# Optimization experiments

Measured on AMD Instinct MI355X. Metric: run time of the kernel, lower is better.

Reference implementation:

```python
import jax, jax.numpy as jnp
import numpy as np

B, H, W, C = 64, 28, 28, 384
NH, WS = 12, 7
KD = C // NH            # key_dim = head_dim = 32 (attn_ratio=1.0 -> d = KD)
QKV_OUT = 3 * KD * NH   # 1152
HID = 4 * C             # mlp hidden
N = WS * WS             # tokens per window
L = H * W
SCALE = KD ** -0.5
EPS_LN = 1e-5
EPS_BN = 1e-5


def _make_bias_idxs():
    pts = [(i, j) for i in range(WS) for j in range(WS)]
    offs, idxs = {}, []
    for p1 in pts:
        for p2 in pts:
            o = (abs(p1[0] - p2[0]), abs(p1[1] - p2[1]))
            if o not in offs:
                offs[o] = len(offs)
            idxs.append(offs[o])
    return np.asarray(idxs, dtype=np.int32).reshape(N, N)


def _ln(x, g, b):
    m = jnp.mean(x, axis=-1, keepdims=True)
    v = jnp.mean(jnp.square(x - m), axis=-1, keepdims=True)
    return (x - m) * jax.lax.rsqrt(v + EPS_LN) * g + b


def setup_inputs() -> dict:
    key = jax.random.key(0)
    ks = jax.random.split(key, 8)
    s = 0.02
    return {
        "x": jax.random.normal(ks[0], (B, L, C), jnp.float32),
        "ln_a_g": jnp.ones((C,), jnp.float32),
        "ln_a_b": jnp.zeros((C,), jnp.float32),
        "qkv_w": jax.random.normal(ks[1], (QKV_OUT, C), jnp.float32) * s,
        "qkv_b": jnp.zeros((QKV_OUT,), jnp.float32),
        "attn_bias": jax.random.normal(ks[2], (NH, N), jnp.float32) * s,
        "proj_w": jax.random.normal(ks[3], (C, C), jnp.float32) * s,
        "proj_b": jnp.zeros((C,), jnp.float32),
        "conv_w": jax.random.normal(ks[4], (C, 1, 3, 3), jnp.float32) * s,
        "bn_g": jnp.ones((C,), jnp.float32),
        "bn_b": jnp.zeros((C,), jnp.float32),
        "bn_m": jnp.zeros((C,), jnp.float32),
        "bn_v": jnp.ones((C,), jnp.float32),
        "ln_m_g": jnp.ones((C,), jnp.float32),
        "ln_m_b": jnp.zeros((C,), jnp.float32),
        "fc1_w": jax.random.normal(ks[5], (HID, C), jnp.float32) * s,
        "fc1_b": jnp.zeros((HID,), jnp.float32),
        "fc2_w": jax.random.normal(ks[6], (C, HID), jnp.float32) * s,
        "fc2_b": jnp.zeros((C,), jnp.float32),
        "bias_idxs": jnp.asarray(_make_bias_idxs()),
    }


def reference(x, ln_a_g, ln_a_b, qkv_w, qkv_b, attn_bias, proj_w, proj_b,
              conv_w, bn_g, bn_b, bn_m, bn_v, ln_m_g, ln_m_b,
              fc1_w, fc1_b, fc2_w, fc2_b, bias_idxs):
    res = x
    nh, nw = H // WS, W // WS
    # window partition: [B,L,C] -> [B*nWin, N, C]
    xw = x.reshape(B, nh, WS, nw, WS, C).transpose(0, 1, 3, 2, 4, 5)
    xw = xw.reshape(B * nh * nw, N, C)
    # attention
    xn = _ln(xw, ln_a_g, ln_a_b)
    qkv = xn @ qkv_w.T + qkv_b                       # [Bw, N, 3*NH*KD]
    qkv = qkv.reshape(-1, N, NH, 3 * KD).transpose(0, 2, 1, 3)
    q, k, v = qkv[..., :KD], qkv[..., KD:2 * KD], qkv[..., 2 * KD:]
    bias = attn_bias[:, bias_idxs]                   # [NH, N, N]
    attn = jnp.einsum('bhnd,bhmd->bhnm', q, k) * SCALE + bias
    attn = jax.nn.softmax(attn, axis=-1)
    o = jnp.einsum('bhnm,bhmd->bhnd', attn, v)
    o = o.transpose(0, 2, 1, 3).reshape(-1, N, C)
    o = o @ proj_w.T + proj_b
    # window unpartition -> [B, L, C]
    o = o.reshape(B, nh, nw, WS, WS, C).transpose(0, 1, 3, 2, 4, 5).reshape(B, L, C)
    x = res + o
    # depthwise ConvBN (inference BN)
    xc = x.transpose(0, 2, 1).reshape(B, C, H, W)
    xc = jax.lax.conv_general_dilated(
        xc, conv_w, (1, 1), 'SAME', feature_group_count=C,
        dimension_numbers=('NCHW', 'OIHW', 'NCHW'))
    inv = jax.lax.rsqrt(bn_v + EPS_BN)
    xc = (xc - bn_m[None, :, None, None]) * (bn_g * inv)[None, :, None, None] + bn_b[None, :, None, None]
    x = xc.reshape(B, C, L).transpose(0, 2, 1)
    # MLP residual
    h = _ln(x, ln_m_g, ln_m_b)
    h = jax.nn.gelu(h @ fc1_w.T + fc1_b, approximate=False)
    h = h @ fc2_w.T + fc2_b
    return x + h
```

## Files before the change

kernel.cpp:

```cpp
#include <hip/hip_runtime.h>
#include <hip/hip_bf16.h>
#include <stdint.h>

#define BATCH 64
#define CC 384
#define NHEAD 12
#define KD 32
#define NTOK 49
#define LL 784
#define MTOT 50176
#define HID 1536
#define QKV_OUT 1152
#define SCALE 0.17677669529663687f
#define EPS 1e-5f

typedef __bf16 bf16x8 __attribute__((ext_vector_type(8)));
typedef float f32x4 __attribute__((ext_vector_type(4)));

__device__ __forceinline__ float bf2f(unsigned short u) {
  union { unsigned int u; float f; } cv; cv.u = ((unsigned int)u) << 16; return cv.f;
}
__device__ __forceinline__ unsigned short f2bf(float f) {
  union { float f; unsigned int u; } cv; cv.f = f;
  unsigned int r = cv.u + 0x7FFFu + ((cv.u >> 16) & 1u);
  return (unsigned short)(r >> 16);
}
__device__ __forceinline__ void gl_lds16(const unsigned short* g, unsigned short* l) {
  __builtin_amdgcn_global_load_lds(
      (const __attribute__((address_space(1))) unsigned int*)g,
      (__attribute__((address_space(3))) unsigned int*)l, 16, 0, 0);
}

__global__ void detect_kernel(const unsigned short* __restrict__ x, int* flag) {
  __shared__ int cnt;
  if (threadIdx.x == 0) cnt = 0;
  __syncthreads();
  int c = 0;
  for (int i = threadIdx.x; i < 4096; i += 256) {
    if (((x[i] >> 7) & 0xFF) == 0xFF) c++;
  }
  atomicAdd(&cnt, c);
  __syncthreads();
  if (threadIdx.x == 0) *flag = (cnt > 0) ? 1 : 0;
}

struct CvtArgs {
  const void* src[19];
  unsigned int n[19];
  unsigned int off[19];
};
__global__ __launch_bounds__(256) void convert_kernel(
    CvtArgs a, unsigned short* __restrict__ dst, const int* __restrict__ flag) {
  const int which = blockIdx.y;
  const unsigned int nn = a.n[which];
  unsigned short* d = dst + a.off[which];
  const unsigned int stride = gridDim.x * blockDim.x;
  const unsigned int idx = blockIdx.x * blockDim.x + threadIdx.x;
  const unsigned int ng = nn >> 3;
  if (*flag) {
    const float* s = (const float*)a.src[which];
    for (unsigned int g = idx; g < ng; g += stride) {
      const float4 f0 = ((const float4*)s)[g * 2];
      const float4 f1 = ((const float4*)s)[g * 2 + 1];
      ushort4 lo, hi;
      lo.x = f2bf(f0.x); lo.y = f2bf(f0.y); lo.z = f2bf(f0.z); lo.w = f2bf(f0.w);
      hi.x = f2bf(f1.x); hi.y = f2bf(f1.y); hi.z = f2bf(f1.z); hi.w = f2bf(f1.w);
      ((ushort4*)d)[g * 2] = lo;
      ((ushort4*)d)[g * 2 + 1] = hi;
    }
    for (unsigned int i = ng * 8 + idx; i < nn; i += stride) d[i] = f2bf(s[i]);
  } else {
    const unsigned short* s = (const unsigned short*)a.src[which];
    for (unsigned int g = idx; g < ng; g += stride)
      ((uint4*)d)[g] = ((const uint4*)s)[g];
    for (unsigned int i = ng * 8 + idx; i < nn; i += stride) d[i] = s[i];
  }
}

__global__ __launch_bounds__(256) void bias_kernel(
    const unsigned short* __restrict__ cAb, const int* __restrict__ bias_idxs,
    float* __restrict__ bias_full) {
  const int h = blockIdx.x;
  for (int i = threadIdx.x; i < NTOK * NTOK; i += 256)
    bias_full[h * NTOK * NTOK + i] = bf2f(cAb[h * NTOK + bias_idxs[i]]);
}

__global__ __launch_bounds__(384) void prep_kernel(
    const unsigned short* __restrict__ cw, const unsigned short* __restrict__ bg,
    const unsigned short* __restrict__ bb, const unsigned short* __restrict__ bm,
    const unsigned short* __restrict__ bv,
    unsigned short* __restrict__ cwT, float* __restrict__ bnsc, float* __restrict__ bnsh) {
  const int c = threadIdx.x;
  const float sc = bf2f(bg[c]) * rsqrtf(bf2f(bv[c]) + EPS);
  bnsc[c] = sc;
  bnsh[c] = bf2f(bb[c]) - bf2f(bm[c]) * sc;
  #pragma unroll
  for (int t = 0; t < 9; ++t) cwT[t * CC + c] = cw[c * 9 + t];
}

__global__ __launch_bounds__(128) void ln_kernel(
    const unsigned short* __restrict__ x, const unsigned short* __restrict__ g,
    const unsigned short* __restrict__ b, unsigned short* __restrict__ out) {
  const int tid = threadIdx.x;
  int wi = blockIdx.y, n = blockIdx.x;
  int bb = wi >> 4, wb = wi & 15;
  int nh_i = wb >> 2, nw_i = wb & 3;
  int hs = n / 7, wsx = n - hs * 7;
  int l = nh_i * 196 + hs * 28 + nw_i * 7 + wsx;
  size_t src_row = (size_t)bb * LL + l;
  size_t dst_row = (size_t)wi * NTOK + n;
  const unsigned short* xr = x + src_row * CC;
  float vals[3]; float s = 0.f, sq = 0.f;
  for (int j = 0; j < 3; ++j) {
    vals[j] = bf2f(xr[tid + 128 * j]);
    s += vals[j]; sq += vals[j] * vals[j];
  }
  for (int off = 32; off; off >>= 1) { s += __shfl_xor(s, off); sq += __shfl_xor(sq, off); }
  __shared__ float red[4];
  const int wv = tid >> 6;
  if ((tid & 63) == 0) { red[wv] = s; red[2 + wv] = sq; }
  __syncthreads();
  float tot = red[0] + red[1], totq = red[2] + red[3];
  float mean = tot * (1.f / CC);
  float var = totq * (1.f / CC) - mean * mean;
  float inv = rsqrtf(var + EPS);
  unsigned short* orow = out + dst_row * CC;
  for (int j = 0; j < 3; ++j) {
    int c = tid + 128 * j;
    float y = (vals[j] - mean) * inv * bf2f(g[c]) + bf2f(b[c]);
    orow[c] = f2bf(y);
  }
}

enum { EP_PLAIN = 0, EP_GELU = 1, EP_WINRES = 2, EP_RES2 = 3 };

template <int EP>
__global__ __launch_bounds__(256) void gemm128(
    const unsigned short* __restrict__ A, const unsigned short* __restrict__ W,
    const unsigned short* __restrict__ bias, const unsigned short* __restrict__ res,
    void* __restrict__ outp, int K, int N, int m_off, const int* __restrict__ flagp) {
  __shared__ __align__(16) unsigned short lds[3 * 8192];
  const int tid = threadIdx.x;
  const int lane = tid & 63;
  const int wave = tid >> 6;
  const int bm = blockIdx.x * 128;
  const int bn = blockIdx.y * 128;
  const int wm = (wave >> 1) * 64;
  const int wn = (wave & 1) * 64;
  const int srow = tid >> 2;
  const int scol = (tid & 3) * 8;
  const unsigned short* Ap0 = A + (size_t)(bm + srow) * K + scol;
  const unsigned short* Wp0 = W + (size_t)(bn + srow) * K + scol;
  const size_t rstep = (size_t)64 * K;
  f32x4 acc[4][4] = {};
  const int kq = (lane >> 4) * 8;
  const int fr = lane & 15;
  const int nt = K >> 5;

  auto stage = [&](int bsel, int t) {
    const unsigned short* ap = Ap0 + t * 32;
    const unsigned short* wp = Wp0 + t * 32;
    unsigned short* al = lds + bsel * 8192 + tid * 8;
    unsigned short* bl = al + 4096;
    gl_lds16(ap, al);
    gl_lds16(ap + rstep, al + 2048);
    gl_lds16(wp, bl);
    gl_lds16(wp + rstep, bl + 2048);
  };

  stage(0, 0);
  stage(1, 1);
  int b = 0;
  for (int t = 0; t < nt; ++t) {
    if (t + 2 < nt) stage(b ? b - 1 : 2, t + 2);
    if (t + 3 <= nt)      asm volatile("s_waitcnt vmcnt(8)" ::: "memory");
    else if (t + 2 == nt) asm volatile("s_waitcnt vmcnt(4)" ::: "memory");
    else                  asm volatile("s_waitcnt vmcnt(0)" ::: "memory");
    __builtin_amdgcn_s_barrier();
    __builtin_amdgcn_sched_barrier(0);
    const unsigned short* Ab = lds + b * 8192;
    const unsigned short* Bb = Ab + 4096;
    bf16x8 af[4], bfr[4];
    #pragma unroll
    for (int i = 0; i < 4; ++i) {
      af[i]  = *(const bf16x8*)(Ab + (wm + i * 16 + fr) * 32 + kq);
      bfr[i] = *(const bf16x8*)(Bb + (wn + i * 16 + fr) * 32 + kq);
    }
    #pragma unroll
    for (int i = 0; i < 4; ++i)
      #pragma unroll
      for (int j = 0; j < 4; ++j)
        acc[i][j] = __builtin_amdgcn_mfma_f32_16x16x32_bf16(af[i], bfr[j], acc[i][j], 0, 0, 0);
    asm volatile("s_waitcnt lgkmcnt(0)" ::: "memory");
    __builtin_amdgcn_sched_barrier(0);
    __builtin_amdgcn_s_barrier();
    b = (b == 2) ? 0 : b + 1;
  }

  int isf32 = 0;
  if (EP == EP_RES2) isf32 = *flagp;
  const int qr = (lane >> 4) * 4;
  float bvs[4];
  #pragma unroll
  for (int tj = 0; tj < 4; ++tj) bvs[tj] = bf2f(bias[bn + wn + tj * 16 + fr]);
  #pragma unroll
  for (int ti = 0; ti < 4; ++ti) {
    #pragma unroll
    for (int r = 0; r < 4; ++r) {
      const int mr = bm + wm + ti * 16 + qr + r;
      size_t rowbase;
      if (EP == EP_WINRES) {
        int wi = mr / 49; int nt2 = mr - wi * 49;
        int bb = wi >> 4; int wb = wi & 15;
        int nh_i = wb >> 2; int nw_i = wb & 3;
        int hs = nt2 / 7; int wsx = nt2 - hs * 7;
        int l = nh_i * 196 + hs * 28 + nw_i * 7 + wsx;
        rowbase = ((size_t)bb * LL + l) * CC;
      } else if (EP == EP_RES2) {
        rowbase = (size_t)(mr + m_off) * N;
      } else {
        rowbase = (size_t)mr * N;
      }
      #pragma unroll
      for (int tj = 0; tj < 4; ++tj) {
        const int n = bn + wn + tj * 16 + fr;
        float v = acc[ti][tj][r] + bvs[tj];
        if (EP == EP_GELU) {
          const float t2 = v * (1.5957691216f + 0.0713548162f * v * v);
          v = __fdividef(v, 1.0f + __expf(-t2));
          ((unsigned short*)outp)[rowbase + n] = f2bf(v);
        } else if (EP == EP_WINRES) {
          size_t idx = rowbase + n;
          v += bf2f(res[idx]);
          ((unsigned short*)outp)[idx] = f2bf(v);
        } else if (EP == EP_RES2) {
          size_t idx = rowbase + n;
          v += bf2f(res[idx]);
          if (isf32) ((float*)outp)[idx] = v;
          else       ((unsigned short*)outp)[idx] = f2bf(v);
        } else {
          ((unsigned short*)outp)[rowbase + n] = f2bf(v);
        }
      }
    }
  }
}

__global__ __launch_bounds__(64) void attn_mfma(
    const unsigned short* __restrict__ qkv, const float* __restrict__ bias_full,
    unsigned short* __restrict__ o, int wi_off) {
  __shared__ __align__(16) unsigned short Pl[64 * 72];
  __shared__ __align__(16) unsigned short vT[32 * 72];
  const int wi = blockIdx.x, h = blockIdx.y;
  const int lane = threadIdx.x;
  const int l15 = lane & 15;
  const int quad = lane >> 4;
  const unsigned short* base = qkv + (size_t)wi * NTOK * QKV_OUT + h * 96;

  bf16x8 qf[4], kf[4];
  #pragma unroll
  for (int i = 0; i < 4; ++i) {
    const int n = i * 16 + l15;
    if (n < NTOK) {
      const unsigned short* p = base + (size_t)n * QKV_OUT + quad * 8;
      qf[i] = *(const bf16x8*)(p);
      kf[i] = *(const bf16x8*)(p + 32);
    } else {
      qf[i] = (bf16x8)0; kf[i] = (bf16x8)0;
    }
  }

  for (int idx = lane; idx < 32 * 72; idx += 64) vT[idx] = 0;
  __syncthreads();
  for (int idx = lane; idx < NTOK * KD; idx += 64) {
    const int m = idx >> 5, d = idx & 31;
    vT[d * 72 + m] = base[(size_t)m * QKV_OUT + 64 + d];
  }

  f32x4 acc[4][4] = {};
  #pragma unroll
  for (int i = 0; i < 4; ++i)
    #pragma unroll
    for (int j = 0; j < 4; ++j)
      acc[i][j] = __builtin_amdgcn_mfma_f32_16x16x32_bf16(qf[i], kf[j], acc[i][j], 0, 0, 0);

  const float* bh = bias_full + h * NTOK * NTOK;
  float rinv[4][4];
  #pragma unroll
  for (int i = 0; i < 4; ++i) {
    #pragma unroll
    for (int r = 0; r < 4; ++r) {
      const int n = i * 16 + quad * 4 + r;
      float sv[4];
      #pragma unroll
      for (int j = 0; j < 4; ++j) {
        const int m = j * 16 + l15;
        float s = acc[i][j][r] * SCALE;
        if (n < NTOK && m < NTOK) s += bh[n * NTOK + m];
        if (m >= NTOK) s = -1e30f;
        sv[j] = s;
      }
      float mx = fmaxf(fmaxf(sv[0], sv[1]), fmaxf(sv[2], sv[3]));
      #pragma unroll
      for (int t = 1; t < 16; t <<= 1) mx = fmaxf(mx, __shfl_xor(mx, t));
      float sum = 0.f;
      #pragma unroll
      for (int j = 0; j < 4; ++j) {
        const float p = __expf(sv[j] - mx);
        sum += p;
        Pl[n * 72 + j * 16 + l15] = f2bf(p);
      }
      #pragma unroll
      for (int t = 1; t < 16; t <<= 1) sum += __shfl_xor(sum, t);
      rinv[i][r] = 1.f / sum;
    }
  }
  __syncthreads();

  f32x4 acc2[4][2] = {};
  #pragma unroll
  for (int kk = 0; kk < 2; ++kk) {
    bf16x8 pf[4], vf[2];
    #pragma unroll
    for (int i = 0; i < 4; ++i)
      pf[i] = *(const bf16x8*)(Pl + (i * 16 + l15) * 72 + kk * 32 + quad * 8);
    #pragma unroll
    for (int jd = 0; jd < 2; ++jd)
      vf[jd] = *(const bf16x8*)(vT + (jd * 16 + l15) * 72 + kk * 32 + quad * 8);
    #pragma unroll
    for (int i = 0; i < 4; ++i)
      #pragma unroll
      for (int jd = 0; jd < 2; ++jd)
        acc2[i][jd] = __builtin_amdgcn_mfma_f32_16x16x32_bf16(pf[i], vf[jd], acc2[i][jd], 0, 0, 0);
  }

  #pragma unroll
  for (int i = 0; i < 4; ++i) {
    #pragma unroll
    for (int r = 0; r < 4; ++r) {
      const int n = i * 16 + quad * 4 + r;
      if (n < NTOK) {
        const float ri = rinv[i][r];
        #pragma unroll
        for (int jd = 0; jd < 2; ++jd) {
          const int d = jd * 16 + l15;
          o[((size_t)(wi_off + wi) * NTOK + n) * CC + h * KD + d] = f2bf(acc2[i][jd][r] * ri);
        }
      }
    }
  }
}

__global__ __launch_bounds__(384) void conv_bn_ln(
    const unsigned short* __restrict__ x1, const unsigned short* __restrict__ cwT,
    const float* __restrict__ bnsc, const float* __restrict__ bnsh,
    const unsigned short* __restrict__ mg, const unsigned short* __restrict__ mb,
    unsigned short* __restrict__ x2, unsigned short* __restrict__ xm) {
  __shared__ float rs[8][48], rq[8][48];
  const int tid = threadIdx.x;
  const int pos = tid / 48;
  const int c8 = tid - pos * 48;
  const int c0 = c8 * 8;
  const int hw = blockIdx.x * 8 + pos;
  const int b = blockIdx.y;
  const int h = hw / 28, w = hw - h * 28;
  float acc[8] = {};
  #pragma unroll
  for (int t = 0; t < 9; ++t) {
    const int dh = t / 3 - 1, dw = t % 3 - 1;
    const int hh = h + dh, ww = w + dw;
    if (hh >= 0 && hh < 28 && ww >= 0 && ww < 28) {
      const uint4 xv = *(const uint4*)(x1 + ((size_t)b * LL + hh * 28 + ww) * CC + c0);
      const uint4 wv = *(const uint4*)(cwT + t * CC + c0);
      const unsigned short* xp = (const unsigned short*)&xv;
      const unsigned short* wp = (const unsigned short*)&wv;
      #pragma unroll
      for (int k = 0; k < 8; ++k) acc[k] += bf2f(xp[k]) * bf2f(wp[k]);
    }
  }
  const float4 sc0 = *(const float4*)(bnsc + c0);
  const float4 sc1 = *(const float4*)(bnsc + c0 + 4);
  const float4 sh0 = *(const float4*)(bnsh + c0);
  const float4 sh1 = *(const float4*)(bnsh + c0 + 4);
  float y[8];
  y[0] = acc[0] * sc0.x + sh0.x; y[1] = acc[1] * sc0.y + sh0.y;
  y[2] = acc[2] * sc0.z + sh0.z; y[3] = acc[3] * sc0.w + sh0.w;
  y[4] = acc[4] * sc1.x + sh1.x; y[5] = acc[5] * sc1.y + sh1.y;
  y[6] = acc[6] * sc1.z + sh1.z; y[7] = acc[7] * sc1.w + sh1.w;
  ushort4 pk0, pk1;
  pk0.x = f2bf(y[0]); pk0.y = f2bf(y[1]); pk0.z = f2bf(y[2]); pk0.w = f2bf(y[3]);
  pk1.x = f2bf(y[4]); pk1.y = f2bf(y[5]); pk1.z = f2bf(y[6]); pk1.w = f2bf(y[7]);
  const size_t row = ((size_t)b * LL + hw) * CC + c0;
  *(ushort4*)(x2 + row) = pk0;
  *(ushort4*)(x2 + row + 4) = pk1;
  float s = 0.f, q = 0.f;
  #pragma unroll
  for (int k = 0; k < 8; ++k) { s += y[k]; q += y[k] * y[k]; }
  rs[pos][c8] = s; rq[pos][c8] = q;
  __syncthreads();
  float tot = 0.f, tq = 0.f;
  #pragma unroll 8
  for (int i = 0; i < 48; ++i) { tot += rs[pos][i]; tq += rq[pos][i]; }
  const float mean = tot * (1.f / CC);
  const float var = tq * (1.f / CC) - mean * mean;
  const float inv = rsqrtf(var + EPS);
  const uint4 gv = *(const uint4*)(mg + c0);
  const uint4 bv = *(const uint4*)(mb + c0);
  const unsigned short* gp = (const unsigned short*)&gv;
  const unsigned short* bp = (const unsigned short*)&bv;
  ushort4 lo, hi;
  unsigned short outv[8];
  #pragma unroll
  for (int k = 0; k < 8; ++k)
    outv[k] = f2bf((y[k] - mean) * inv * bf2f(gp[k]) + bf2f(bp[k]));
  lo.x = outv[0]; lo.y = outv[1]; lo.z = outv[2]; lo.w = outv[3];
  hi.x = outv[4]; hi.y = outv[5]; hi.z = outv[6]; hi.w = outv[7];
  *(ushort4*)(xm + row) = lo;
  *(ushort4*)(xm + row + 4) = hi;
}

extern "C" void kernel_launch(void* const* d_in, const int* in_sizes, int n_in,
                              void* d_out, int out_size, void* d_ws, size_t ws_size,
                              hipStream_t stream) {
  int* flag = (int*)d_ws;
  unsigned short* base = (unsigned short*)d_ws;

  CvtArgs args;
  size_t cur = 32;
  size_t off[19];
  for (int i = 0; i < 19; ++i) {
    off[i] = cur;
    args.src[i] = d_in[i];
    args.n[i] = (unsigned int)in_sizes[i];
    args.off[i] = (unsigned int)cur;
    cur += ((size_t)in_sizes[i] + 63) & ~(size_t)63;
  }
  const unsigned short* cx   = base + off[0];
  const unsigned short* cgA  = base + off[1];
  const unsigned short* cbA  = base + off[2];
  const unsigned short* cQw  = base + off[3];
  const unsigned short* cQb  = base + off[4];
  const unsigned short* cAb  = base + off[5];
  const unsigned short* cPw  = base + off[6];
  const unsigned short* cPb  = base + off[7];
  const unsigned short* cCw  = base + off[8];
  const unsigned short* cBg  = base + off[9];
  const unsigned short* cBb  = base + off[10];
  const unsigned short* cBm  = base + off[11];
  const unsigned short* cBv  = base + off[12];
  const unsigned short* cMg  = base + off[13];
  const unsigned short* cMb  = base + off[14];
  const unsigned short* cF1w = base + off[15];
  const unsigned short* cF1b = base + off[16];
  const unsigned short* cF2w = base + off[17];
  const unsigned short* cF2b = base + off[18];
  const int* bias_idxs = (const int*)d_in[19];

  const size_t SZ = (size_t)MTOT * CC;
  unsigned short* o_buf = base + cur;
  unsigned short* buf2  = o_buf + SZ;
  unsigned short* x2    = base + off[0];
  float* bias_full = (float*)(buf2 + (size_t)25088 * HID);
  unsigned short* cwT = (unsigned short*)(bias_full + 12 * NTOK * NTOK);
  float* bnsc = (float*)(cwT + 9 * CC + ((9 * CC) & 7 ? 0 : 0));
  float* bnsh = bnsc + CC;

  unsigned short* xn = (unsigned short*)d_out;

  detect_kernel<<<1, 256, 0, stream>>>((const unsigned short*)d_in[0], flag);
  convert_kernel<<<dim3(512, 19), 256, 0, stream>>>(args, base, flag);
  bias_kernel<<<NHEAD, 256, 0, stream>>>(cAb, bias_idxs, bias_full);
  prep_kernel<<<1, 384, 0, stream>>>(cCw, cBg, cBb, cBm, cBv, cwT, bnsc, bnsh);

  ln_kernel<<<dim3(49, 1024), 128, 0, stream>>>(cx, cgA, cbA, xn);

  for (int half = 0; half < 2; ++half) {
    gemm128<EP_PLAIN><<<dim3(196, 9), 256, 0, stream>>>(
        xn + (size_t)half * 25088 * CC, cQw, cQb, nullptr, buf2, CC, QKV_OUT, 0, nullptr);
    attn_mfma<<<dim3(512, NHEAD), 64, 0, stream>>>(buf2, bias_full, o_buf, half * 512);
  }

  gemm128<EP_WINRES><<<dim3(392, 3), 256, 0, stream>>>(
      o_buf, cPw, cPb, cx, d_out, CC, CC, 0, nullptr);

  conv_bn_ln<<<dim3(98, BATCH), 384, 0, stream>>>(
      (const unsigned short*)d_out, cwT, bnsc, bnsh, cMg, cMb, x2, o_buf);

  for (int half = 0; half < 2; ++half) {
    gemm128<EP_GELU><<<dim3(196, 12), 256, 0, stream>>>(
        o_buf + (size_t)half * 25088 * CC, cF1w, cF1b, nullptr, buf2, CC, HID, 0, nullptr);
    gemm128<EP_RES2><<<dim3(196, 3), 256, 0, stream>>>(
        buf2, cF2w, cF2b, x2, d_out, HID, CC, half * 25088, flag);
  }
}
```

Baseline: 733.1 us.

## Use BK=64 XOR-swizzled double-buffered GEMM tiles and single-chunk launches

The GEMM main loop goes from a triple-buffered 32-wide K tile to a double-buffered 64-wide K tile. The LDS columns are XOR-swizzled to avoid bank conflicts on the fragment reads. This halves the number of barrier and wait iterations per tile and gives two MFMAs per fragment pair. The host side also drops the fixed two-half split of the QKV/attention and MLP phases when the workspace is large enough, launching one larger grid instead, at the cost of a larger intermediate buffer.

Result: slower. 769.9 us (+5.0%).

```diff
diff --git a/kernel.cpp b/kernel.cpp
--- a/kernel.cpp
+++ b/kernel.cpp
@@ -139,7 +139,7 @@
     const unsigned short* __restrict__ A, const unsigned short* __restrict__ W,
     const unsigned short* __restrict__ bias, const unsigned short* __restrict__ res,
     void* __restrict__ outp, int K, int N, int m_off, const int* __restrict__ flagp) {
-  __shared__ __align__(16) unsigned short lds[3 * 8192];
+  __shared__ __align__(16) unsigned short lds[2 * 16384];
   const int tid = threadIdx.x;
   const int lane = tid & 63;
   const int wave = tid >> 6;
@@ -147,54 +147,64 @@
   const int bn = blockIdx.y * 128;
   const int wm = (wave >> 1) * 64;
   const int wn = (wave & 1) * 64;
-  const int srow = tid >> 2;
-  const int scol = (tid & 3) * 8;
-  const unsigned short* Ap0 = A + (size_t)(bm + srow) * K + scol;
-  const unsigned short* Wp0 = W + (size_t)(bn + srow) * K + scol;
-  const size_t rstep = (size_t)64 * K;
+  const int g_row = tid >> 3;
+  const int g_c   = tid & 7;
+  const int s_col = (g_c ^ (g_row & 7)) * 8;
+  const unsigned short* Ap0 = A + (size_t)(bm + g_row) * K + s_col;
+  const unsigned short* Wp0 = W + (size_t)(bn + g_row) * K + s_col;
+  const size_t rstep32 = (size_t)32 * K;
   f32x4 acc[4][4] = {};
-  const int kq = (lane >> 4) * 8;
   const int fr = lane & 15;
-  const int nt = K >> 5;
+  const int quad = lane >> 4;
+  const int nt = K >> 6;
+  const int rs_a = (wm + fr) * 64;
+  const int rs_b = (wn + fr) * 64;
+  const int cg0 = (quad ^ (fr & 7)) * 8;
+  const int cg1 = ((4 + quad) ^ (fr & 7)) * 8;
 
   auto stage = [&](int bsel, int t) {
-    const unsigned short* ap = Ap0 + t * 32;
-    const unsigned short* wp = Wp0 + t * 32;
-    unsigned short* al = lds + bsel * 8192 + tid * 8;
-    unsigned short* bl = al + 4096;
-    gl_lds16(ap, al);
-    gl_lds16(ap + rstep, al + 2048);
-    gl_lds16(wp, bl);
-    gl_lds16(wp + rstep, bl + 2048);
+    const unsigned short* ap = Ap0 + (size_t)t * 64;
+    const unsigned short* wp = Wp0 + (size_t)t * 64;
+    unsigned short* al = lds + bsel * 16384 + tid * 8;
+    unsigned short* bl = al + 8192;
+    #pragma unroll
+    for (int j = 0; j < 4; ++j) {
+      gl_lds16(ap + j * rstep32, al + j * 2048);
+      gl_lds16(wp + j * rstep32, bl + j * 2048);
+    }
   };
 
   stage(0, 0);
-  stage(1, 1);
-  int b = 0;
   for (int t = 0; t < nt; ++t) {
-    if (t + 2 < nt) stage(b ? b - 1 : 2, t + 2);
-    if (t + 3 <= nt)      asm volatile("s_waitcnt vmcnt(8)" ::: "memory");
-    else if (t + 2 == nt) asm volatile("s_waitcnt vmcnt(4)" ::: "memory");
-    else                  asm volatile("s_waitcnt vmcnt(0)" ::: "memory");
+    const int cb = t & 1;
+    if (t + 1 < nt) {
+      stage(cb ^ 1, t + 1);
+      asm volatile("s_waitcnt vmcnt(8)" ::: "memory");
+    } else {
+      asm volatile("s_waitcnt vmcnt(0)" ::: "memory");
+    }
     __builtin_amdgcn_s_barrier();
     __builtin_amdgcn_sched_barrier(0);
-    const unsigned short* Ab = lds + b * 8192;
-    const unsigned short* Bb = Ab + 4096;
-    bf16x8 af[4], bfr[4];
+    const unsigned short* Ab = lds + cb * 16384;
+    const unsigned short* Bb = Ab + 8192;
+    bf16x8 af0[4], af1[4], bf0[4], bf1[4];
     #pragma unroll
     for (int i = 0; i < 4; ++i) {
-      af[i]  = *(const bf16x8*)(Ab + (wm + i * 16 + fr) * 32 + kq);
-      bfr[i] = *(const bf16x8*)(Bb + (wn + i * 16 + fr) * 32 + kq);
+      af0[i] = *(const bf16x8*)(Ab + rs_a + i * 1024 + cg0);
+      af1[i] = *(const bf16x8*)(Ab + rs_a + i * 1024 + cg1);
+      bf0[i] = *(const bf16x8*)(Bb + rs_b + i * 1024 + cg0);
+      bf1[i] = *(const bf16x8*)(Bb + rs_b + i * 1024 + cg1);
     }
     #pragma unroll
     for (int i = 0; i < 4; ++i)
       #pragma unroll
-      for (int j = 0; j < 4; ++j)
-        acc[i][j] = __builtin_amdgcn_mfma_f32_16x16x32_bf16(af[i], bfr[j], acc[i][j], 0, 0, 0);
+      for (int j = 0; j < 4; ++j) {
+        acc[i][j] = __builtin_amdgcn_mfma_f32_16x16x32_bf16(af0[i], bf0[j], acc[i][j], 0, 0, 0);
+        acc[i][j] = __builtin_amdgcn_mfma_f32_16x16x32_bf16(af1[i], bf1[j], acc[i][j], 0, 0, 0);
+      }
     asm volatile("s_waitcnt lgkmcnt(0)" ::: "memory");
     __builtin_amdgcn_sched_barrier(0);
     __builtin_amdgcn_s_barrier();
-    b = (b == 2) ? 0 : b + 1;
   }
 
   int isf32 = 0;
@@ -457,12 +467,19 @@
   const int* bias_idxs = (const int*)d_in[19];
 
   const size_t SZ = (size_t)MTOT * CC;
+  const size_t need_full_bytes =
+      (cur + SZ + (size_t)MTOT * HID) * 2 + 512 * 1024;
+  const int nchunk = (ws_size >= need_full_bytes) ? 1 : 2;
+  const int MC = MTOT / nchunk;
+  const int WC = 1024 / nchunk;
+  const size_t buf2_cap = (size_t)MC * HID;
+
   unsigned short* o_buf = base + cur;
   unsigned short* buf2  = o_buf + SZ;
   unsigned short* x2    = base + off[0];
-  float* bias_full = (float*)(buf2 + (size_t)25088 * HID);
+  float* bias_full = (float*)(buf2 + buf2_cap);
   unsigned short* cwT = (unsigned short*)(bias_full + 12 * NTOK * NTOK);
-  float* bnsc = (float*)(cwT + 9 * CC + ((9 * CC) & 7 ? 0 : 0));
+  float* bnsc = (float*)(cwT + 9 * CC);
   float* bnsh = bnsc + CC;
 
   unsigned short* xn = (unsigned short*)d_out;
@@ -474,22 +491,22 @@
 
   ln_kernel<<<dim3(49, 1024), 128, 0, stream>>>(cx, cgA, cbA, xn);
 
-  for (int half = 0; half < 2; ++half) {
-    gemm128<EP_PLAIN><<<dim3(196, 9), 256, 0, stream>>>(
-        xn + (size_t)half * 25088 * CC, cQw, cQb, nullptr, buf2, CC, QKV_OUT, 0, nullptr);
-    attn_mfma<<<dim3(512, NHEAD), 64, 0, stream>>>(buf2, bias_full, o_buf, half * 512);
-  }
-
-  gemm128<EP_WINRES><<<dim3(392, 3), 256, 0, stream>>>(
+  for (int c = 0; c < nchunk; ++c) {
+    gemm128<EP_PLAIN><<<dim3(MC / 128, QKV_OUT / 128), 256, 0, stream>>>(
+        xn + (size_t)c * MC * CC, cQw, cQb, nullptr, buf2, CC, QKV_OUT, 0, nullptr);
+    attn_mfma<<<dim3(WC, NHEAD), 64, 0, stream>>>(buf2, bias_full, o_buf, c * WC);
+  }
+
+  gemm128<EP_WINRES><<<dim3(MTOT / 128, CC / 128), 256, 0, stream>>>(
       o_buf, cPw, cPb, cx, d_out, CC, CC, 0, nullptr);
 
   conv_bn_ln<<<dim3(98, BATCH), 384, 0, stream>>>(
       (const unsigned short*)d_out, cwT, bnsc, bnsh, cMg, cMb, x2, o_buf);
 
-  for (int half = 0; half < 2; ++half) {
-    gemm128<EP_GELU><<<dim3(196, 12), 256, 0, stream>>>(
-        o_buf + (size_t)half * 25088 * CC, cF1w, cF1b, nullptr, buf2, CC, HID, 0, nullptr);
-    gemm128<EP_RES2><<<dim3(196, 3), 256, 0, stream>>>(
-        buf2, cF2w, cF2b, x2, d_out, HID, CC, half * 25088, flag);
-  }
-}
+  for (int c = 0; c < nchunk; ++c) {
+    gemm128<EP_GELU><<<dim3(MC / 128, HID / 128), 256, 0, stream>>>(
+        o_buf + (size_t)c * MC * CC, cF1w, cF1b, nullptr, buf2, CC, HID, 0, nullptr);
+    gemm128<EP_RES2><<<dim3(MC / 128, CC / 128), 256, 0, stream>>>(
+        buf2, cF2w, cF2b, x2, d_out, HID, CC, c * MC, flag);
+  }
+}
```

## Add XCD-aware tile remap, LDS XOR swizzle, and single-chunk launch when workspace allows

Applied to the files above, without the earlier changes.

The GEMM grid becomes 1D and is remapped so that consecutive tile IDs land on the same XCD, with M-major ordering so tiles that share A/W rows stay in the same L2. Global-to-LDS staging and the fragment reads now use an XOR swizzle on the 8-element column group, which is meant to cut LDS bank conflicts. The host also checks whether the workspace can hold the full MLP hidden buffer and, if so, runs the QKV/attention and FC1/FC2 stages in one chunk instead of two, which removes launches and tail effects. The risk is that the workspace-size check or the swizzle index math could be subtly wrong.

Measured after the change: 670.0 us. -8.6%, faster.

```diff
diff --git a/kernel.cpp b/kernel.cpp
--- a/kernel.cpp
+++ b/kernel.cpp
@@ -138,28 +138,35 @@
 __global__ __launch_bounds__(256) void gemm128(
     const unsigned short* __restrict__ A, const unsigned short* __restrict__ W,
     const unsigned short* __restrict__ bias, const unsigned short* __restrict__ res,
-    void* __restrict__ outp, int K, int N, int m_off, const int* __restrict__ flagp) {
+    void* __restrict__ outp, int K, int N, int m_off, const int* __restrict__ flagp,
+    int Nt) {
   __shared__ __align__(16) unsigned short lds[3 * 8192];
   const int tid = threadIdx.x;
   const int lane = tid & 63;
   const int wave = tid >> 6;
-  const int bm = blockIdx.x * 128;
-  const int bn = blockIdx.y * 128;
+  const int nwg = gridDim.x;
+  const int id = blockIdx.x;
+  const int q8 = nwg >> 3, r8 = nwg & 7;
+  const int xcd = id & 7, rank = id >> 3;
+  const int wgid = (xcd < r8 ? xcd * (q8 + 1) : r8 * (q8 + 1) + (xcd - r8) * q8) + rank;
+  const int bm = (wgid / Nt) * 128;
+  const int bn = (wgid - (wgid / Nt) * Nt) * 128;
   const int wm = (wave >> 1) * 64;
   const int wn = (wave & 1) * 64;
   const int srow = tid >> 2;
-  const int scol = (tid & 3) * 8;
-  const unsigned short* Ap0 = A + (size_t)(bm + srow) * K + scol;
-  const unsigned short* Wp0 = W + (size_t)(bn + srow) * K + scol;
+  const int s_col = ((tid & 3) ^ (srow & 3)) * 8;
+  const unsigned short* Ap0 = A + (size_t)(bm + srow) * K + s_col;
+  const unsigned short* Wp0 = W + (size_t)(bn + srow) * K + s_col;
   const size_t rstep = (size_t)64 * K;
   f32x4 acc[4][4] = {};
-  const int kq = (lane >> 4) * 8;
   const int fr = lane & 15;
+  const int quad = lane >> 4;
   const int nt = K >> 5;
+  const int cg = (quad ^ (fr & 3)) * 8;
 
   auto stage = [&](int bsel, int t) {
-    const unsigned short* ap = Ap0 + t * 32;
-    const unsigned short* wp = Wp0 + t * 32;
+    const unsigned short* ap = Ap0 + (size_t)t * 32;
+    const unsigned short* wp = Wp0 + (size_t)t * 32;
     unsigned short* al = lds + bsel * 8192 + tid * 8;
     unsigned short* bl = al + 4096;
     gl_lds16(ap, al);
@@ -183,8 +190,8 @@
     bf16x8 af[4], bfr[4];
     #pragma unroll
     for (int i = 0; i < 4; ++i) {
-      af[i]  = *(const bf16x8*)(Ab + (wm + i * 16 + fr) * 32 + kq);
-      bfr[i] = *(const bf16x8*)(Bb + (wn + i * 16 + fr) * 32 + kq);
+      af[i]  = *(const bf16x8*)(Ab + (wm + i * 16 + fr) * 32 + cg);
+      bfr[i] = *(const bf16x8*)(Bb + (wn + i * 16 + fr) * 32 + cg);
     }
     #pragma unroll
     for (int i = 0; i < 4; ++i)
@@ -457,12 +464,19 @@
   const int* bias_idxs = (const int*)d_in[19];
 
   const size_t SZ = (size_t)MTOT * CC;
+  const size_t need_full_bytes =
+      (cur + SZ + (size_t)MTOT * HID) * 2 + 512 * 1024;
+  const int nchunk = (ws_size >= need_full_bytes) ? 1 : 2;
+  const int MC = MTOT / nchunk;
+  const int WC = 1024 / nchunk;
+  const size_t buf2_cap = (size_t)MC * HID;
+
   unsigned short* o_buf = base + cur;
   unsigned short* buf2  = o_buf + SZ;
   unsigned short* x2    = base + off[0];
-  float* bias_full = (float*)(buf2 + (size_t)25088 * HID);
+  float* bias_full = (float*)(buf2 + buf2_cap);
   unsigned short* cwT = (unsigned short*)(bias_full + 12 * NTOK * NTOK);
-  float* bnsc = (float*)(cwT + 9 * CC + ((9 * CC) & 7 ? 0 : 0));
+  float* bnsc = (float*)(cwT + 9 * CC);
   float* bnsh = bnsc + CC;
 
   unsigned short* xn = (unsigned short*)d_out;
@@ -474,22 +488,24 @@
 
   ln_kernel<<<dim3(49, 1024), 128, 0, stream>>>(cx, cgA, cbA, xn);
 
-  for (int half = 0; half < 2; ++half) {
-    gemm128<EP_PLAIN><<<dim3(196, 9), 256, 0, stream>>>(
-        xn + (size_t)half * 25088 * CC, cQw, cQb, nullptr, buf2, CC, QKV_OUT, 0, nullptr);
-    attn_mfma<<<dim3(512, NHEAD), 64, 0, stream>>>(buf2, bias_full, o_buf, half * 512);
-  }
-
-  gemm128<EP_WINRES><<<dim3(392, 3), 256, 0, stream>>>(
-      o_buf, cPw, cPb, cx, d_out, CC, CC, 0, nullptr);
+  for (int c = 0; c < nchunk; ++c) {
+    gemm128<EP_PLAIN><<<(MC / 128) * (QKV_OUT / 128), 256, 0, stream>>>(
+        xn + (size_t)c * MC * CC, cQw, cQb, nullptr, buf2, CC, QKV_OUT, 0, nullptr,
+        QKV_OUT / 128);
+    attn_mfma<<<dim3(WC, NHEAD), 64, 0, stream>>>(buf2, bias_full, o_buf, c * WC);
+  }
+
+  gemm128<EP_WINRES><<<(MTOT / 128) * (CC / 128), 256, 0, stream>>>(
+      o_buf, cPw, cPb, cx, d_out, CC, CC, 0, nullptr, CC / 128);
 
   conv_bn_ln<<<dim3(98, BATCH), 384, 0, stream>>>(
       (const unsigned short*)d_out, cwT, bnsc, bnsh, cMg, cMb, x2, o_buf);
 
-  for (int half = 0; half < 2; ++half) {
-    gemm128<EP_GELU><<<dim3(196, 12), 256, 0, stream>>>(
-        o_buf + (size_t)half * 25088 * CC, cF1w, cF1b, nullptr, buf2, CC, HID, 0, nullptr);
-    gemm128<EP_RES2><<<dim3(196, 3), 256, 0, stream>>>(
-        buf2, cF2w, cF2b, x2, d_out, HID, CC, half * 25088, flag);
-  }
-}
+  for (int c = 0; c < nchunk; ++c) {
+    gemm128<EP_GELU><<<(MC / 128) * (HID / 128), 256, 0, stream>>>(
+        o_buf + (size_t)c * MC * CC, cF1w, cF1b, nullptr, buf2, CC, HID, 0, nullptr,
+        HID / 128);
+    gemm128<EP_RES2><<<(MC / 128) * (CC / 128), 256, 0, stream>>>(
+        buf2, cF2w, cF2b, x2, d_out, HID, CC, c * MC, flag, CC / 128);
+  }
+}
```
